# Kernel optimization log

Measured on AMD Instinct MI355X. Metric: run time of the kernel, lower is better.

## Reference

```python
import jax, jax.numpy as jnp
import numpy as np
import math

CHUNK = 256
NUM_HEADS = 4
EPS = 1e-5


def setup_inputs() -> dict:
    key = jax.random.key(0)
    ks = jax.random.split(key, 12)
    B, N, F = 4, 2048, 256
    x = jax.random.normal(ks[0], (B, N, F), dtype=jnp.float32)
    adj_matrix = jax.random.randint(ks[1], (N, N), 0, 2, dtype=jnp.int32)
    s = 1.0 / math.sqrt(F)
    Wq = jax.random.normal(ks[2], (F, F), dtype=jnp.float32) * s
    bq = jnp.zeros((F,), dtype=jnp.float32)
    Wk = jax.random.normal(ks[3], (F, F), dtype=jnp.float32) * s
    bk = jnp.zeros((F,), dtype=jnp.float32)
    Wv = jax.random.normal(ks[4], (F, F), dtype=jnp.float32) * s
    bv = jnp.zeros((F,), dtype=jnp.float32)
    Wo = jax.random.normal(ks[5], (F, F), dtype=jnp.float32) * s
    bo = jnp.zeros((F,), dtype=jnp.float32)
    gamma = jnp.ones((F,), dtype=jnp.float32)
    beta = jnp.zeros((F,), dtype=jnp.float32)
    return {"x": x, "adj_matrix": adj_matrix, "Wq": Wq, "bq": bq, "Wk": Wk,
            "bk": bk, "Wv": Wv, "bv": bv, "Wo": Wo, "bo": bo,
            "gamma": gamma, "beta": beta}


def reference(x, adj_matrix, Wq, bq, Wk, bk, Wv, bv, Wo, bo, gamma, beta):
    B, N, Fin = x.shape
    H = NUM_HEADS
    Dout = Wq.shape[0]
    Dh = Dout // H
    Nc = N // CHUNK  # number of key chunks

    # projections -> [B, H, N, Dh]
    q = (x @ Wq.T + bq).reshape(B, N, H, Dh).transpose(0, 2, 1, 3)
    k = (x @ Wk.T + bk).reshape(B, N, H, Dh).transpose(0, 2, 1, 3)
    v = (x @ Wv.T + bv).reshape(B, N, H, Dh).transpose(0, 2, 1, 3)

    # key/value chunks: [B, H, Nc, CHUNK, Dh]
    kc = k.reshape(B, H, Nc, CHUNK, Dh)
    vc = v.reshape(B, H, Nc, CHUNK, Dh)

    # scores per key chunk: [B, H, N, Nc, CHUNK]
    scores = jnp.einsum('bhnd,bhjcd->bhnjc', q, kc) / jnp.sqrt(
        jnp.asarray(Dh, dtype=q.dtype))
    scores = jnp.clip(scores, -10.0, 10.0)
    # adjacency mask, chunked along keys: [1, 1, N, Nc, CHUNK]
    mask = adj_matrix.reshape(N, Nc, CHUNK)[None, None]
    scores = jnp.where(mask == 0, jnp.asarray(-10.0, scores.dtype), scores)

    # FAITHFUL quirk: softmax is taken per key chunk (last axis only) and the
    # per-chunk contexts are SUMMED -> total attention mass per query is Nc.
    attn = jax.nn.softmax(scores, axis=-1)
    ctx = jnp.einsum('bhnjc,bhjcd->bhnd', attn, vc)  # sum over chunks j

    ctx = ctx.transpose(0, 2, 1, 3).reshape(B, N, Dout)
    out = ctx @ Wo.T + bo
    out = out + x  # residual (in_features == out_features)

    mu = jnp.mean(out, axis=-1, keepdims=True)
    var = jnp.mean(jnp.square(out - mu), axis=-1, keepdims=True)
    out = (out - mu) * jax.lax.rsqrt(var + EPS) * gamma + beta
    return out
```

## Files before the change

kernel.cpp:

```cpp
#include <hip/hip_runtime.h>
#include <math.h>

#define B_     4
#define N_     2048
#define F_     256
#define H_     4
#define DH     64
#define NC     8
#define BN     8192
#define SP     72

typedef _Float16 f16;
typedef _Float16 half8  __attribute__((ext_vector_type(8)));
typedef _Float16 half4v __attribute__((ext_vector_type(4)));
typedef float    floatx4 __attribute__((ext_vector_type(4)));
typedef unsigned long long u64;

__device__ __forceinline__ half8 cvt8(float4 a, float4 b) {
    half8 h;
    h[0] = (f16)a.x; h[1] = (f16)a.y; h[2] = (f16)a.z; h[3] = (f16)a.w;
    h[4] = (f16)b.x; h[5] = (f16)b.y; h[6] = (f16)b.z; h[7] = (f16)b.w;
    return h;
}

__global__ __launch_bounds__(256) void pack_adj(
    const int* __restrict__ adj, u64* __restrict__ P)
{
    const int row   = blockIdx.x >> 3;
    const int chunk = blockIdx.x & 7;
    const int wave  = threadIdx.x >> 6, lane = threadIdx.x & 63;
    const int key   = chunk * 256 + wave * 64 + lane;
    u64 m = __ballot(adj[(size_t)row * N_ + key] != 0);
    if (lane == 0) P[(size_t)row * 32 + chunk * 4 + wave] = m;
}

__global__ __launch_bounds__(256) void proj_mfma(
    const float* __restrict__ x,
    const float* __restrict__ Wq, const float* __restrict__ Wk, const float* __restrict__ Wv,
    const float* __restrict__ bq, const float* __restrict__ bk, const float* __restrict__ bv,
    f16* __restrict__ Qh, f16* __restrict__ Kh, f16* __restrict__ Vt)
{
    const int which = blockIdx.z;
    const float* W    = which == 0 ? Wq : which == 1 ? Wk : Wv;
    const float* bias = which == 0 ? bq : which == 1 ? bk : bv;

    const int r0 = blockIdx.x * 64;
    const int hy = blockIdx.y;
    const int c0 = hy * 64;
    const int tid  = threadIdx.x;
    const int wave = tid >> 6, lane = tid & 63;
    const int quad = lane >> 4, l16 = lane & 15;
    const int row = tid >> 2, seg = tid & 3;

    __shared__ f16 xs[64 * SP];
    __shared__ f16 wsm[64 * SP];

    floatx4 zz = {0.f, 0.f, 0.f, 0.f};
    floatx4 acc[4] = {zz, zz, zz, zz};

    for (int f0 = 0; f0 < F_; f0 += 64) {
        const float* xsrc = x + (size_t)(r0 + row) * F_ + f0 + seg * 16;
        const float* wsrc = W + (size_t)(c0 + row) * F_ + f0 + seg * 16;
        float4 xa0 = *(const float4*)(xsrc + 0), xa1 = *(const float4*)(xsrc + 4);
        float4 xa2 = *(const float4*)(xsrc + 8), xa3 = *(const float4*)(xsrc + 12);
        float4 wa0 = *(const float4*)(wsrc + 0), wa1 = *(const float4*)(wsrc + 4);
        float4 wa2 = *(const float4*)(wsrc + 8), wa3 = *(const float4*)(wsrc + 12);
        __syncthreads();
        *(half8*)&xs[row * SP + seg * 16]      = cvt8(xa0, xa1);
        *(half8*)&xs[row * SP + seg * 16 + 8]  = cvt8(xa2, xa3);
        *(half8*)&wsm[row * SP + seg * 16]     = cvt8(wa0, wa1);
        *(half8*)&wsm[row * SP + seg * 16 + 8] = cvt8(wa2, wa3);
        __syncthreads();
#pragma unroll
        for (int s = 0; s < 2; s++) {
            half8 af = *(const half8*)&xs[(wave * 16 + l16) * SP + s * 32 + quad * 8];
#pragma unroll
            for (int ot = 0; ot < 4; ot++) {
                half8 bf = *(const half8*)&wsm[(ot * 16 + l16) * SP + s * 32 + quad * 8];
                acc[ot] = __builtin_amdgcn_mfma_f32_16x16x32_f16(af, bf, acc[ot], 0, 0, 0);
            }
        }
    }

    const int bb = r0 >> 11, nn0 = r0 & (N_ - 1);

    if (which == 2) {
#pragma unroll
        for (int ot = 0; ot < 4; ot++) {
            const float bv_ = bias[c0 + ot * 16 + l16];
            half4v h4;
#pragma unroll
            for (int r = 0; r < 4; r++) h4[r] = (f16)(acc[ot][r] + bv_);
            *(half4v*)(Vt + (((size_t)bb * H_ + hy) * DH + ot * 16 + l16) * N_
                          + nn0 + wave * 16 + quad * 4) = h4;
        }
    } else {
        f16* dst = which == 0 ? Qh : Kh;
        __syncthreads();
        f16* outb = xs;
#pragma unroll
        for (int ot = 0; ot < 4; ot++) {
            const float bv_ = bias[c0 + ot * 16 + l16];
#pragma unroll
            for (int r = 0; r < 4; r++)
                outb[(wave * 16 + quad * 4 + r) * SP + ot * 16 + l16] = (f16)(acc[ot][r] + bv_);
        }
        __syncthreads();
        f16* g = dst + (((size_t)bb * H_ + hy) * N_ + nn0 + row) * DH + seg * 16;
        *(float4*)(g)     = *(const float4*)&outb[row * SP + seg * 16];
        *(float4*)(g + 8) = *(const float4*)&outb[row * SP + seg * 16 + 8];
    }
}

__global__ __launch_bounds__(256) void attn_mfma(
    const f16* __restrict__ Qh, const f16* __restrict__ Kh,
    const f16* __restrict__ Vt, const u64* __restrict__ Padj,
    f16* __restrict__ CTXP)
{
    const int nt = blockIdx.x & 31;
    const int sp = blockIdx.x >> 5;
    const int qb = nt * 64;
    const int h  = blockIdx.y;
    const int b  = blockIdx.z;
    const int bh = b * H_ + h;
    const int tid  = threadIdx.x;
    const int wave = tid >> 6, lane = tid & 63;
    const int quad = lane >> 4, l16 = lane & 15;
    const int row = tid >> 2, seg = tid & 3;

    __shared__ f16 QPs[64 * SP];
    __shared__ f16 Ks[64 * SP];
    __shared__ f16 Vs[64 * SP];

    {
        const f16* src = Qh + ((size_t)bh * N_ + qb + row) * DH + seg * 16;
        *(float4*)&QPs[row * SP + seg * 16]     = *(const float4*)(src);
        *(float4*)&QPs[row * SP + seg * 16 + 8] = *(const float4*)(src + 8);
    }
    __syncthreads();
    const half8 qf0 = *(const half8*)&QPs[(wave * 16 + l16) * SP + quad * 8];
    const half8 qf1 = *(const half8*)&QPs[(wave * 16 + l16) * SP + 32 + quad * 8];
    f16* Ps = QPs + wave * 16 * SP;

    const int qglob = qb + wave * 16 + l16;
    const u64* arow = Padj + (size_t)qglob * 32;

    floatx4 zz = {0.f, 0.f, 0.f, 0.f};
    floatx4 ctx_tot[4] = {zz, zz, zz, zz};

    for (int ci = 0; ci < 2; ci++) {
        const int c = sp * 2 + ci;
        floatx4 ctx_ch[4] = {zz, zz, zz, zz};
        float rs_ch = 0.f;

        for (int kt = 0; kt < 4; kt++) {
            const int k0 = c * 256 + kt * 64;
            const f16* ksrc = Kh + ((size_t)bh * N_ + k0 + row) * DH + seg * 16;
            const f16* vsrc = Vt + ((size_t)bh * DH + row) * N_ + k0 + seg * 16;
            float4 ka0 = *(const float4*)(ksrc), ka1 = *(const float4*)(ksrc + 8);
            float4 va0 = *(const float4*)(vsrc), va1 = *(const float4*)(vsrc + 8);
            __syncthreads();
            *(float4*)&Ks[row * SP + seg * 16]     = ka0;
            *(float4*)&Ks[row * SP + seg * 16 + 8] = ka1;
            *(float4*)&Vs[row * SP + seg * 16]     = va0;
            *(float4*)&Vs[row * SP + seg * 16 + 8] = va1;
            __syncthreads();

            const u64 aw = arow[k0 >> 6];
            float rs = 0.f;
#pragma unroll
            for (int m = 0; m < 4; m++) {
                floatx4 sacc = zz;
                half8 a0 = *(const half8*)&Ks[(m * 16 + l16) * SP + quad * 8];
                half8 a1 = *(const half8*)&Ks[(m * 16 + l16) * SP + 32 + quad * 8];
                sacc = __builtin_amdgcn_mfma_f32_16x16x32_f16(a0, qf0, sacc, 0, 0, 0);
                sacc = __builtin_amdgcn_mfma_f32_16x16x32_f16(a1, qf1, sacc, 0, 0, 0);
                const unsigned int nib = (unsigned int)(aw >> (m * 16 + quad * 4)) & 0xFu;
                half4v pv;
#pragma unroll
                for (int r = 0; r < 4; r++) {
                    float sv = sacc[r] * 0.125f;
                    sv = fminf(fmaxf(sv, -10.f), 10.f);
                    sv = ((nib >> r) & 1u) ? sv : -10.f;
                    const float ev = __expf(sv);
                    rs += ev;
                    pv[r] = (f16)ev;
                }
                *(half4v*)&Ps[l16 * SP + m * 16 + quad * 4] = pv;
            }
            rs += __shfl_xor(rs, 16);
            rs += __shfl_xor(rs, 32);
            rs_ch += rs;

            const half8 p0 = *(const half8*)&Ps[l16 * SP + quad * 8];
            const half8 p1 = *(const half8*)&Ps[l16 * SP + 32 + quad * 8];
#pragma unroll
            for (int m = 0; m < 4; m++) {
                half8 va = *(const half8*)&Vs[(m * 16 + l16) * SP + quad * 8];
                half8 vb = *(const half8*)&Vs[(m * 16 + l16) * SP + 32 + quad * 8];
                ctx_ch[m] = __builtin_amdgcn_mfma_f32_16x16x32_f16(va, p0, ctx_ch[m], 0, 0, 0);
                ctx_ch[m] = __builtin_amdgcn_mfma_f32_16x16x32_f16(vb, p1, ctx_ch[m], 0, 0, 0);
            }
        }

        const float inv = 1.0f / rs_ch;
#pragma unroll
        for (int m = 0; m < 4; m++)
#pragma unroll
            for (int r = 0; r < 4; r++)
                ctx_tot[m][r] += ctx_ch[m][r] * inv;
    }

    f16* dst = CTXP + (((size_t)sp * B_ + b) * N_ + qglob) * F_ + h * DH;
#pragma unroll
    for (int m = 0; m < 4; m++) {
        half4v h4;
#pragma unroll
        for (int r = 0; r < 4; r++) h4[r] = (f16)ctx_tot[m][r];
        *(half4v*)&dst[m * 16 + quad * 4] = h4;
    }
}

__global__ __launch_bounds__(256) void sum_ctx(
    const f16* __restrict__ CTXP, float* __restrict__ CTX)
{
    const size_t S = (size_t)BN * F_;
    const size_t i = ((size_t)blockIdx.x * 256 + threadIdx.x) * 8;
    half8 a0 = *(const half8*)(CTXP + i);
    half8 a1 = *(const half8*)(CTXP + S + i);
    half8 a2 = *(const half8*)(CTXP + 2 * S + i);
    half8 a3 = *(const half8*)(CTXP + 3 * S + i);
    float4 o0, o1;
    o0.x = (float)a0[0] + (float)a1[0] + (float)a2[0] + (float)a3[0];
    o0.y = (float)a0[1] + (float)a1[1] + (float)a2[1] + (float)a3[1];
    o0.z = (float)a0[2] + (float)a1[2] + (float)a2[2] + (float)a3[2];
    o0.w = (float)a0[3] + (float)a1[3] + (float)a2[3] + (float)a3[3];
    o1.x = (float)a0[4] + (float)a1[4] + (float)a2[4] + (float)a3[4];
    o1.y = (float)a0[5] + (float)a1[5] + (float)a2[5] + (float)a3[5];
    o1.z = (float)a0[6] + (float)a1[6] + (float)a2[6] + (float)a3[6];
    o1.w = (float)a0[7] + (float)a1[7] + (float)a2[7] + (float)a3[7];
    *(float4*)(CTX + i)     = o0;
    *(float4*)(CTX + i + 4) = o1;
}

__global__ __launch_bounds__(256) void transpose_wo(
    const float* __restrict__ Wo, float* __restrict__ WoT)
{
    const int idx = blockIdx.x * 256 + threadIdx.x;
    const int f = idx >> 8;
    const int o = idx & 255;
    WoT[(size_t)f * F_ + o] = Wo[(size_t)o * F_ + f];
}

__global__ __launch_bounds__(256) void out_ln_kernel(
    const float* __restrict__ CTX, const float* __restrict__ x,
    const float* __restrict__ WoT, const float* __restrict__ bo,
    const float* __restrict__ gamma, const float* __restrict__ beta,
    float* __restrict__ out)
{
    const int n0 = blockIdx.x * 4;
    const int o  = threadIdx.x;

    float acc[4] = {0.f, 0.f, 0.f, 0.f};
    for (int f = 0; f < F_; f += 4) {
        const float w0 = WoT[(size_t)(f + 0) * F_ + o];
        const float w1 = WoT[(size_t)(f + 1) * F_ + o];
        const float w2 = WoT[(size_t)(f + 2) * F_ + o];
        const float w3 = WoT[(size_t)(f + 3) * F_ + o];
#pragma unroll
        for (int r = 0; r < 4; r++) {
            float4 c4 = *(const float4*)(CTX + (size_t)(n0 + r) * F_ + f);
            acc[r] += c4.x * w0 + c4.y * w1 + c4.z * w2 + c4.w * w3;
        }
    }

    float ov[4];
#pragma unroll
    for (int r = 0; r < 4; r++)
        ov[r] = acc[r] + bo[o] + x[(size_t)(n0 + r) * F_ + o];

    __shared__ float psum[4][4], psq[4][4];
    const int wave = o >> 6, lane = o & 63;
#pragma unroll
    for (int r = 0; r < 4; r++) {
        float sv = ov[r], qv = ov[r] * ov[r];
#pragma unroll
        for (int off = 1; off < 64; off <<= 1) {
            sv += __shfl_xor(sv, off);
            qv += __shfl_xor(qv, off);
        }
        if (lane == 0) { psum[wave][r] = sv; psq[wave][r] = qv; }
    }
    __syncthreads();
#pragma unroll
    for (int r = 0; r < 4; r++) {
        const float S  = (psum[0][r] + psum[1][r]) + (psum[2][r] + psum[3][r]);
        const float Q2 = (psq[0][r] + psq[1][r]) + (psq[2][r] + psq[3][r]);
        const float mu  = S * (1.0f / F_);
        const float var = Q2 * (1.0f / F_) - mu * mu;
        const float inv = rsqrtf(var + 1e-5f);
        out[(size_t)(n0 + r) * F_ + o] = (ov[r] - mu) * inv * gamma[o] + beta[o];
    }
}

extern "C" void kernel_launch(void* const* d_in, const int* in_sizes, int n_in,
                              void* d_out, int out_size, void* d_ws, size_t ws_size,
                              hipStream_t stream)
{
    const float* x     = (const float*)d_in[0];
    const int*   adj   = (const int*)  d_in[1];
    const float* Wq    = (const float*)d_in[2];
    const float* bq    = (const float*)d_in[3];
    const float* Wk    = (const float*)d_in[4];
    const float* bk    = (const float*)d_in[5];
    const float* Wv    = (const float*)d_in[6];
    const float* bv    = (const float*)d_in[7];
    const float* Wo    = (const float*)d_in[8];
    const float* bo    = (const float*)d_in[9];
    const float* gamma = (const float*)d_in[10];
    const float* beta  = (const float*)d_in[11];
    float* out = (float*)d_out;

    float* ws = (float*)d_ws;
    float* WoT  = ws;
    f16*   CTXP = (f16*)(ws + 65536);
    f16*   Qh   = (f16*)(ws + 4259840);
    f16*   Kh   = (f16*)(ws + 5308416);
    f16*   Vt   = (f16*)(ws + 6356992);
    u64*   Padj = (u64*)(ws + 7405568);
    float* CTX  = (float*)Qh;

    hipLaunchKernelGGL(pack_adj, dim3(N_ * 8), dim3(256), 0, stream, adj, Padj);
    hipLaunchKernelGGL(proj_mfma, dim3(BN / 64, H_, 3), dim3(256), 0, stream,
                       x, Wq, Wk, Wv, bq, bk, bv, Qh, Kh, Vt);
    hipLaunchKernelGGL(transpose_wo, dim3((F_ * F_) / 256), dim3(256), 0, stream,
                       Wo, WoT);
    hipLaunchKernelGGL(attn_mfma, dim3(128, H_, B_), dim3(256), 0, stream,
                       Qh, Kh, Vt, Padj, CTXP);
    hipLaunchKernelGGL(sum_ctx, dim3(1024), dim3(256), 0, stream, CTXP, CTX);
    hipLaunchKernelGGL(out_ln_kernel, dim3(BN / 4), dim3(256), 0, stream,
                       CTX, x, WoT, bo, gamma, beta, out);
}
```

Baseline: 186.8 us.

## Fuse ctx sum into MFMA output-projection+LN, fold scale into Q, drop LDS staging in attention

Replaces the scalar fp32 output projection and LayerNorm kernel with an MFMA fp16 kernel that also sums the four partial context buffers, which removes the separate sum_ctx and transpose kernels. Folds the 1/sqrt(Dh) and log2(e) factors into Q at projection time so attention can use exp2 directly. Attention now reads K and V fragments straight from global memory instead of staging them through shared memory, dropping two barriers per tile. The cost is redundant global or L2 traffic across waves in attention, and fp16 rounding of Wo and of the summed context.

Measured after the change: 249.6 us. 33.7% more time.

```diff
diff --git a/kernel.cpp b/kernel.cpp
--- a/kernel.cpp
+++ b/kernel.cpp
@@ -6,9 +6,12 @@
 #define F_     256
 #define H_     4
 #define DH     64
-#define NC     8
 #define BN     8192
 #define SP     72
+#define SPW    264
+
+#define QSCALE 0.18033688011112042f
+#define CLIP   14.426950408889634f
 
 typedef _Float16 f16;
 typedef _Float16 half8  __attribute__((ext_vector_type(8)));
@@ -32,6 +35,15 @@
     const int key   = chunk * 256 + wave * 64 + lane;
     u64 m = __ballot(adj[(size_t)row * N_ + key] != 0);
     if (lane == 0) P[(size_t)row * 32 + chunk * 4 + wave] = m;
+}
+
+__global__ __launch_bounds__(256) void cvt_wo(
+    const float* __restrict__ Wo, f16* __restrict__ Woh)
+{
+    const int idx = (blockIdx.x * 256 + threadIdx.x) * 4;
+    float4 v = *(const float4*)(Wo + idx);
+    half4v h; h[0] = (f16)v.x; h[1] = (f16)v.y; h[2] = (f16)v.z; h[3] = (f16)v.w;
+    *(half4v*)(Woh + idx) = h;
 }
 
 __global__ __launch_bounds__(256) void proj_mfma(
@@ -95,6 +107,7 @@
                           + nn0 + wave * 16 + quad * 4) = h4;
         }
     } else {
+        const float scl = (which == 0) ? QSCALE : 1.0f;
         f16* dst = which == 0 ? Qh : Kh;
         __syncthreads();
         f16* outb = xs;
@@ -103,7 +116,8 @@
             const float bv_ = bias[c0 + ot * 16 + l16];
 #pragma unroll
             for (int r = 0; r < 4; r++)
-                outb[(wave * 16 + quad * 4 + r) * SP + ot * 16 + l16] = (f16)(acc[ot][r] + bv_);
+                outb[(wave * 16 + quad * 4 + r) * SP + ot * 16 + l16] =
+                    (f16)((acc[ot][r] + bv_) * scl);
         }
         __syncthreads();
         f16* g = dst + (((size_t)bb * H_ + hy) * N_ + nn0 + row) * DH + seg * 16;
@@ -126,21 +140,13 @@
     const int tid  = threadIdx.x;
     const int wave = tid >> 6, lane = tid & 63;
     const int quad = lane >> 4, l16 = lane & 15;
-    const int row = tid >> 2, seg = tid & 3;
-
-    __shared__ f16 QPs[64 * SP];
-    __shared__ f16 Ks[64 * SP];
-    __shared__ f16 Vs[64 * SP];
-
-    {
-        const f16* src = Qh + ((size_t)bh * N_ + qb + row) * DH + seg * 16;
-        *(float4*)&QPs[row * SP + seg * 16]     = *(const float4*)(src);
-        *(float4*)&QPs[row * SP + seg * 16 + 8] = *(const float4*)(src + 8);
-    }
-    __syncthreads();
-    const half8 qf0 = *(const half8*)&QPs[(wave * 16 + l16) * SP + quad * 8];
-    const half8 qf1 = *(const half8*)&QPs[(wave * 16 + l16) * SP + 32 + quad * 8];
-    f16* Ps = QPs + wave * 16 * SP;
+
+    __shared__ f16 Ps[4 * 16 * SP];
+    f16* Psw = Ps + wave * 16 * SP;
+
+    const f16* qbase = Qh + ((size_t)bh * N_ + qb + wave * 16 + l16) * DH + quad * 8;
+    const half8 qf0 = *(const half8*)(qbase);
+    const half8 qf1 = *(const half8*)(qbase + 32);
 
     const int qglob = qb + wave * 16 + l16;
     const u64* arow = Padj + (size_t)qglob * 32;
@@ -155,51 +161,42 @@
 
         for (int kt = 0; kt < 4; kt++) {
             const int k0 = c * 256 + kt * 64;
-            const f16* ksrc = Kh + ((size_t)bh * N_ + k0 + row) * DH + seg * 16;
-            const f16* vsrc = Vt + ((size_t)bh * DH + row) * N_ + k0 + seg * 16;
-            float4 ka0 = *(const float4*)(ksrc), ka1 = *(const float4*)(ksrc + 8);
-            float4 va0 = *(const float4*)(vsrc), va1 = *(const float4*)(vsrc + 8);
-            __syncthreads();
-            *(float4*)&Ks[row * SP + seg * 16]     = ka0;
-            *(float4*)&Ks[row * SP + seg * 16 + 8] = ka1;
-            *(float4*)&Vs[row * SP + seg * 16]     = va0;
-            *(float4*)&Vs[row * SP + seg * 16 + 8] = va1;
-            __syncthreads();
-
             const u64 aw = arow[k0 >> 6];
+            const f16* kb = Kh + ((size_t)bh * N_ + k0 + l16) * DH + quad * 8;
+            const f16* vb = Vt + ((size_t)bh * DH + l16) * N_ + k0 + quad * 8;
+
             float rs = 0.f;
 #pragma unroll
             for (int m = 0; m < 4; m++) {
+                half8 a0 = *(const half8*)(kb + m * 16 * DH);
+                half8 a1 = *(const half8*)(kb + m * 16 * DH + 32);
                 floatx4 sacc = zz;
-                half8 a0 = *(const half8*)&Ks[(m * 16 + l16) * SP + quad * 8];
-                half8 a1 = *(const half8*)&Ks[(m * 16 + l16) * SP + 32 + quad * 8];
                 sacc = __builtin_amdgcn_mfma_f32_16x16x32_f16(a0, qf0, sacc, 0, 0, 0);
                 sacc = __builtin_amdgcn_mfma_f32_16x16x32_f16(a1, qf1, sacc, 0, 0, 0);
                 const unsigned int nib = (unsigned int)(aw >> (m * 16 + quad * 4)) & 0xFu;
                 half4v pv;
 #pragma unroll
                 for (int r = 0; r < 4; r++) {
-                    float sv = sacc[r] * 0.125f;
-                    sv = fminf(fmaxf(sv, -10.f), 10.f);
-                    sv = ((nib >> r) & 1u) ? sv : -10.f;
-                    const float ev = __expf(sv);
+                    float sv = fminf(fmaxf(sacc[r], -CLIP), CLIP);
+                    sv = ((nib >> r) & 1u) ? sv : -CLIP;
+                    const float ev = __builtin_amdgcn_exp2f(sv);
                     rs += ev;
                     pv[r] = (f16)ev;
                 }
-                *(half4v*)&Ps[l16 * SP + m * 16 + quad * 4] = pv;
+                *(half4v*)&Psw[l16 * SP + m * 16 + quad * 4] = pv;
             }
             rs += __shfl_xor(rs, 16);
             rs += __shfl_xor(rs, 32);
             rs_ch += rs;
 
-            const half8 p0 = *(const half8*)&Ps[l16 * SP + quad * 8];
-            const half8 p1 = *(const half8*)&Ps[l16 * SP + 32 + quad * 8];
+            const half8 p0 = *(const half8*)&Psw[l16 * SP + quad * 8];
+            const half8 p1 = *(const half8*)&Psw[l16 * SP + 32 + quad * 8];
 #pragma unroll
             for (int m = 0; m < 4; m++) {
-                half8 va = *(const half8*)&Vs[(m * 16 + l16) * SP + quad * 8];
-                half8 vb = *(const half8*)&Vs[(m * 16 + l16) * SP + 32 + quad * 8];
-                ctx_ch[m] = __builtin_amdgcn_mfma_f32_16x16x32_f16(va, p0, ctx_ch[m], 0, 0, 0);
-                ctx_ch[m] = __builtin_amdgcn_mfma_f32_16x16x32_f16(vb, p1, ctx_ch[m], 0, 0, 0);
+                half8 va  = *(const half8*)(vb + (size_t)(m * 16) * N_);
+                half8 vb8 = *(const half8*)(vb + (size_t)(m * 16) * N_ + 32);
+                ctx_ch[m] = __builtin_amdgcn_mfma_f32_16x16x32_f16(va,  p0, ctx_ch[m], 0, 0, 0);
+                ctx_ch[m] = __builtin_amdgcn_mfma_f32_16x16x32_f16(vb8, p1, ctx_ch[m], 0, 0, 0);
             }
         }
 
@@ -221,85 +218,92 @@
     }
 }
 
-__global__ __launch_bounds__(256) void sum_ctx(
-    const f16* __restrict__ CTXP, float* __restrict__ CTX)
-{
-    const size_t S = (size_t)BN * F_;
-    const size_t i = ((size_t)blockIdx.x * 256 + threadIdx.x) * 8;
-    half8 a0 = *(const half8*)(CTXP + i);
-    half8 a1 = *(const half8*)(CTXP + S + i);
-    half8 a2 = *(const half8*)(CTXP + 2 * S + i);
-    half8 a3 = *(const half8*)(CTXP + 3 * S + i);
-    float4 o0, o1;
-    o0.x = (float)a0[0] + (float)a1[0] + (float)a2[0] + (float)a3[0];
-    o0.y = (float)a0[1] + (float)a1[1] + (float)a2[1] + (float)a3[1];
-    o0.z = (float)a0[2] + (float)a1[2] + (float)a2[2] + (float)a3[2];
-    o0.w = (float)a0[3] + (float)a1[3] + (float)a2[3] + (float)a3[3];
-    o1.x = (float)a0[4] + (float)a1[4] + (float)a2[4] + (float)a3[4];
-    o1.y = (float)a0[5] + (float)a1[5] + (float)a2[5] + (float)a3[5];
-    o1.z = (float)a0[6] + (float)a1[6] + (float)a2[6] + (float)a3[6];
-    o1.w = (float)a0[7] + (float)a1[7] + (float)a2[7] + (float)a3[7];
-    *(float4*)(CTX + i)     = o0;
-    *(float4*)(CTX + i + 4) = o1;
-}
-
-__global__ __launch_bounds__(256) void transpose_wo(
-    const float* __restrict__ Wo, float* __restrict__ WoT)
-{
-    const int idx = blockIdx.x * 256 + threadIdx.x;
-    const int f = idx >> 8;
-    const int o = idx & 255;
-    WoT[(size_t)f * F_ + o] = Wo[(size_t)o * F_ + f];
-}
-
-__global__ __launch_bounds__(256) void out_ln_kernel(
-    const float* __restrict__ CTX, const float* __restrict__ x,
-    const float* __restrict__ WoT, const float* __restrict__ bo,
+__global__ __launch_bounds__(256) void out_mfma(
+    const f16* __restrict__ CTXP, const float* __restrict__ x,
+    const f16* __restrict__ Woh, const float* __restrict__ bo,
     const float* __restrict__ gamma, const float* __restrict__ beta,
     float* __restrict__ out)
 {
-    const int n0 = blockIdx.x * 4;
-    const int o  = threadIdx.x;
-
-    float acc[4] = {0.f, 0.f, 0.f, 0.f};
-    for (int f = 0; f < F_; f += 4) {
-        const float w0 = WoT[(size_t)(f + 0) * F_ + o];
-        const float w1 = WoT[(size_t)(f + 1) * F_ + o];
-        const float w2 = WoT[(size_t)(f + 2) * F_ + o];
-        const float w3 = WoT[(size_t)(f + 3) * F_ + o];
-#pragma unroll
-        for (int r = 0; r < 4; r++) {
-            float4 c4 = *(const float4*)(CTX + (size_t)(n0 + r) * F_ + f);
-            acc[r] += c4.x * w0 + c4.y * w1 + c4.z * w2 + c4.w * w3;
-        }
-    }
-
-    float ov[4];
-#pragma unroll
-    for (int r = 0; r < 4; r++)
-        ov[r] = acc[r] + bo[o] + x[(size_t)(n0 + r) * F_ + o];
-
-    __shared__ float psum[4][4], psq[4][4];
-    const int wave = o >> 6, lane = o & 63;
+    const int n0 = blockIdx.x * 16;
+    const int tid  = threadIdx.x;
+    const int wave = tid >> 6, lane = tid & 63;
+    const int quad = lane >> 4, l16 = lane & 15;
+
+    __shared__ f16 cs[16 * SPW];
+    __shared__ float red0[4][16], red1[4][16];
+
+    {
+        const int row = tid >> 4, c0 = (tid & 15) * 16;
+        const size_t S = (size_t)BN * F_;
+        const f16* p = CTXP + (size_t)(n0 + row) * F_ + c0;
+#pragma unroll
+        for (int g = 0; g < 2; g++) {
+            half8 s0 = *(const half8*)(p + g * 8);
+            half8 s1 = *(const half8*)(p + S + g * 8);
+            half8 s2 = *(const half8*)(p + 2 * S + g * 8);
+            half8 s3 = *(const half8*)(p + 3 * S + g * 8);
+            half8 o;
+#pragma unroll
+            for (int e = 0; e < 8; e++)
+                o[e] = (f16)(((float)s0[e] + (float)s1[e]) + ((float)s2[e] + (float)s3[e]));
+            *(half8*)&cs[row * SPW + c0 + g * 8] = o;
+        }
+    }
+    __syncthreads();
+
+    floatx4 zz = {0.f, 0.f, 0.f, 0.f};
+    floatx4 acc[4] = {zz, zz, zz, zz};
+
+#pragma unroll
+    for (int f0 = 0; f0 < F_; f0 += 64) {
+        half8 a0 = *(const half8*)&cs[l16 * SPW + f0 + quad * 8];
+        half8 a1 = *(const half8*)&cs[l16 * SPW + f0 + 32 + quad * 8];
+#pragma unroll
+        for (int ot = 0; ot < 4; ot++) {
+            const f16* wrow = Woh + (size_t)(wave * 64 + ot * 16 + l16) * F_ + f0 + quad * 8;
+            half8 b0 = *(const half8*)(wrow);
+            half8 b1 = *(const half8*)(wrow + 32);
+            acc[ot] = __builtin_amdgcn_mfma_f32_16x16x32_f16(a0, b0, acc[ot], 0, 0, 0);
+            acc[ot] = __builtin_amdgcn_mfma_f32_16x16x32_f16(a1, b1, acc[ot], 0, 0, 0);
+        }
+    }
+
+#pragma unroll
+    for (int ot = 0; ot < 4; ot++) {
+        const int o = wave * 64 + ot * 16 + l16;
+        const float bo_ = bo[o];
+#pragma unroll
+        for (int r = 0; r < 4; r++)
+            acc[ot][r] += bo_ + x[(size_t)(n0 + quad * 4 + r) * F_ + o];
+    }
+
 #pragma unroll
     for (int r = 0; r < 4; r++) {
-        float sv = ov[r], qv = ov[r] * ov[r];
-#pragma unroll
-        for (int off = 1; off < 64; off <<= 1) {
-            sv += __shfl_xor(sv, off);
-            qv += __shfl_xor(qv, off);
-        }
-        if (lane == 0) { psum[wave][r] = sv; psq[wave][r] = qv; }
+        float s = (acc[0][r] + acc[1][r]) + (acc[2][r] + acc[3][r]);
+        float q = (acc[0][r] * acc[0][r] + acc[1][r] * acc[1][r]) +
+                  (acc[2][r] * acc[2][r] + acc[3][r] * acc[3][r]);
+        s += __shfl_xor(s, 1); q += __shfl_xor(q, 1);
+        s += __shfl_xor(s, 2); q += __shfl_xor(q, 2);
+        s += __shfl_xor(s, 4); q += __shfl_xor(q, 4);
+        s += __shfl_xor(s, 8); q += __shfl_xor(q, 8);
+        if (l16 == 0) { red0[wave][quad * 4 + r] = s; red1[wave][quad * 4 + r] = q; }
     }
     __syncthreads();
+
 #pragma unroll
     for (int r = 0; r < 4; r++) {
-        const float S  = (psum[0][r] + psum[1][r]) + (psum[2][r] + psum[3][r]);
-        const float Q2 = (psq[0][r] + psq[1][r]) + (psq[2][r] + psq[3][r]);
+        const int rr = quad * 4 + r;
+        const float S  = (red0[0][rr] + red0[1][rr]) + (red0[2][rr] + red0[3][rr]);
+        const float Q2 = (red1[0][rr] + red1[1][rr]) + (red1[2][rr] + red1[3][rr]);
         const float mu  = S * (1.0f / F_);
         const float var = Q2 * (1.0f / F_) - mu * mu;
         const float inv = rsqrtf(var + 1e-5f);
-        out[(size_t)(n0 + r) * F_ + o] = (ov[r] - mu) * inv * gamma[o] + beta[o];
+#pragma unroll
+        for (int ot = 0; ot < 4; ot++) {
+            const int o = wave * 64 + ot * 16 + l16;
+            out[(size_t)(n0 + rr) * F_ + o] =
+                (acc[ot][r] - mu) * inv * gamma[o] + beta[o];
+        }
     }
 }
 
@@ -322,22 +326,19 @@
     float* out = (float*)d_out;
 
     float* ws = (float*)d_ws;
-    float* WoT  = ws;
-    f16*   CTXP = (f16*)(ws + 65536);
-    f16*   Qh   = (f16*)(ws + 4259840);
-    f16*   Kh   = (f16*)(ws + 5308416);
-    f16*   Vt   = (f16*)(ws + 6356992);
-    u64*   Padj = (u64*)(ws + 7405568);
-    float* CTX  = (float*)Qh;
+    f16*   CTXP = (f16*)(ws);
+    f16*   Qh   = (f16*)(ws + 4194304);
+    f16*   Kh   = (f16*)(ws + 5242880);
+    f16*   Vt   = (f16*)(ws + 6291456);
+    u64*   Padj = (u64*)(ws + 7340032);
+    f16*   Woh  = (f16*)(ws + 7471104);
 
     hipLaunchKernelGGL(pack_adj, dim3(N_ * 8), dim3(256), 0, stream, adj, Padj);
+    hipLaunchKernelGGL(cvt_wo, dim3(64), dim3(256), 0, stream, Wo, Woh);
     hipLaunchKernelGGL(proj_mfma, dim3(BN / 64, H_, 3), dim3(256), 0, stream,
                        x, Wq, Wk, Wv, bq, bk, bv, Qh, Kh, Vt);
-    hipLaunchKernelGGL(transpose_wo, dim3((F_ * F_) / 256), dim3(256), 0, stream,
-                       Wo, WoT);
     hipLaunchKernelGGL(attn_mfma, dim3(128, H_, B_), dim3(256), 0, stream,
                        Qh, Kh, Vt, Padj, CTXP);
-    hipLaunchKernelGGL(sum_ctx, dim3(1024), dim3(256), 0, stream, CTXP, CTX);
-    hipLaunchKernelGGL(out_ln_kernel, dim3(BN / 4), dim3(256), 0, stream,
-                       CTX, x, WoT, bo, gamma, beta, out);
-}
+    hipLaunchKernelGGL(out_mfma, dim3(BN / 16), dim3(256), 0, stream,
+                       CTXP, x, Woh, bo, gamma, beta, out);
+}
```
